# Kernel optimization log

Hardware: AMD Instinct MI355X
Metric: run time of the kernel (lower is better)

Reference implementation:

```python
import jax, jax.numpy as jnp
import numpy as np


def setup_inputs() -> dict:
    key = jax.random.key(0)
    k1, k2 = jax.random.split(key)
    n_nodes, d_feat, n_edges = 100000, 48, 1600000
    x = jax.random.normal(k1, (n_nodes, d_feat), dtype=jnp.float32)
    edge_index = jax.random.randint(k2, (2, n_edges), 0, n_nodes, dtype=jnp.int64)
    return {"x": x, "edge_index": edge_index, "batch_size": 65536}


def reference(x, edge_index, batch_size):
    # adj = SparseTensor.from_edge_index(edge_index): adj[row, col] = 1 with
    # row = edge_index[0] (src), col = edge_index[1] (dst).
    # adj.t() @ x  ->  out[i] = sum over edges (src -> i) of x[src]
    src, dst = edge_index[0], edge_index[1]
    n_nodes = x.shape[0]
    # memory-bound gather + scatter-add (SpMM, sum aggregation)
    x_neighbors_sum = jax.ops.segment_sum(x[src], dst, num_segments=n_nodes)
    node_labels = jnp.concatenate(
        (x[:batch_size, :], x_neighbors_sum[:batch_size, :]), axis=-1
    )
    return node_labels
```

## Files before the change

### kernel.cpp

```cpp
#include <hip/hip_runtime.h>
#include <hip/hip_fp16.h>

#define DFEAT 48
#define OUTW  96
#define NBINB 1024
#define BINTH 512
#define EPT   4
#define SORTCAP 2048
#define NBUCK2 512
#define RBITS 7
#define NROWS 128
#define RAWCAP 2560
#define CSRCAP 2560


static __device__ __forceinline__ unsigned short f2h(float f) {
    __half h = __float2half_rn(f);
    return *reinterpret_cast<unsigned short*>(&h);
}

static __device__ __forceinline__ int wave_iscan(int v, int lane) {
    #pragma unroll
    for (int d = 1; d < 64; d <<= 1) {
        int tv = __shfl_up(v, d, 64);
        if (lane >= d) v += tv;
    }
    return v;
}

__global__ __launch_bounds__(BINTH)
void bin_k(const int* __restrict__ ei, int n_edges, int batch, int chunk,
           const float4* __restrict__ x4, int nx4, uint2* __restrict__ xh4,
           unsigned short* __restrict__ starts, unsigned int* __restrict__ regions,
           float4* __restrict__ out4, int use_half) {
    __shared__ int cnt[NBUCK2];
    __shared__ int cur[NBUCK2];
    __shared__ int wsum[BINTH / 64];
    __shared__ int totS;
    __shared__ unsigned int sorted[SORTCAP];
    const int t = threadIdx.x;
    const int b = blockIdx.x;
    const int lane = t & 63, wid = t >> 6;

    if (use_half) {
        const int batch12 = batch * 12;
        for (int i = b * BINTH + t; i < nx4; i += NBINB * BINTH) {
            float4 v = x4[i];
            xh4[i] = make_uint2((unsigned)f2h(v.x) | ((unsigned)f2h(v.y) << 16),
                                (unsigned)f2h(v.z) | ((unsigned)f2h(v.w) << 16));
            if (i < batch12) {
                int row = i / 12, cg = i - row * 12;
                out4[(size_t)row * 24 + cg] = v;
            }
        }
    }

    const int beg = b * chunk;
    const int end = min(beg + chunk, n_edges);

    unsigned int pay[EPT];
    int bkt[EPT];
    #pragma unroll
    for (int i = 0; i < EPT; i++) {
        bkt[i] = -1;
        int e = beg + t + i * BINTH;
        if (e < end) {
            int dst = ei[n_edges + e];
            if (dst < batch) {
                int src = ei[e];
                bkt[i] = dst >> RBITS;
                pay[i] = ((unsigned)(dst & (NROWS - 1)) << 17) | (unsigned)src;
            }
        }
    }
    cnt[t] = 0;
    __syncthreads();
    #pragma unroll
    for (int i = 0; i < EPT; i++)
        if (bkt[i] >= 0) atomicAdd(&cnt[bkt[i]], 1);
    __syncthreads();
    int v = cnt[t];
    int iv = wave_iscan(v, lane);
    if (lane == 63) wsum[wid] = iv;
    __syncthreads();
    if (t < BINTH / 64) {
        int wv = wsum[t];
        int sv = wave_iscan(wv, t);
        wsum[t] = sv - wv;
        if (t == BINTH / 64 - 1) totS = sv;
    }
    __syncthreads();
    int excl = iv - v + wsum[wid];
    int tot = totS;
    cur[t] = excl;
    starts[t * NBINB + b] = (unsigned short)excl;
    if (t == 0) starts[NBUCK2 * NBINB + b] = (unsigned short)tot;
    __syncthreads();
    #pragma unroll
    for (int i = 0; i < EPT; i++)
        if (bkt[i] >= 0) {
            int pos = atomicAdd(&cur[bkt[i]], 1);
            sorted[pos] = pay[i];
        }
    __syncthreads();
    unsigned int* reg = regions + (size_t)b * chunk;
    for (int i = t; i < tot; i += BINTH) reg[i] = sorted[i];
}

__global__ __launch_bounds__(1024)
void reduce_k(const float* __restrict__ x, const uint4* __restrict__ xh4,
              const unsigned short* __restrict__ starts,
              const unsigned int* __restrict__ regions,
              float* __restrict__ out, int batch, int chunk, int use_half) {
    __shared__ unsigned int raw[RAWCAP];
    __shared__ int csr[CSRCAP];
    __shared__ int cnt[NROWS], off[NROWS + 1], cur[NROWS];
    __shared__ int rbase[NBINB], rs[NBINB], rl[NBINB];
    __shared__ int wsum[16];
    __shared__ int totS;
    const int t = threadIdx.x;
    const int kb = blockIdx.x;
    const int lane = t & 63, wid = t >> 6;

    int s0 = 0, len = 0;
    if (t < NBINB) {
        s0 = starts[kb * NBINB + t];
        int s1 = starts[(kb + 1) * NBINB + t];
        len = s1 - s0;
    }
    int iv = wave_iscan(len, lane);
    if (lane == 63 && wid < 16) wsum[wid] = iv;
    __syncthreads();
    if (t < 16) {
        int wv = wsum[t];
        int sv = wave_iscan(wv, t);
        wsum[t] = sv - wv;
        if (t == 15) totS = sv;
    }
    __syncthreads();
    if (t < NBINB) {
        rbase[t] = iv - len + wsum[wid];
        rs[t] = s0;
        rl[t] = len;
    }
    __syncthreads();
    const int T = min(totS, RAWCAP);
    {
        int r = t;
        if (r < NBINB) {
            int L = rl[r], base = rbase[r];
            const unsigned int* reg = regions + (size_t)r * chunk + rs[r];
            for (int idx = 0; idx < L; ++idx) {
                int p = base + idx;
                if (p < RAWCAP) raw[p] = reg[idx];
            }
        }
    }
    if (t < NROWS) cnt[t] = 0;
    __syncthreads();
    for (int i = t; i < T; i += 1024) atomicAdd(&cnt[raw[i] >> 17], 1);
    __syncthreads();
    int v2 = (t < NROWS) ? cnt[t] : 0;
    int iv2 = wave_iscan(v2, lane);
    if (lane == 63 && wid < 2) wsum[wid] = iv2;
    __syncthreads();
    if (t == 0) {
        int a = wsum[0];
        off[NROWS] = a + wsum[1];
        wsum[1] = a;
        wsum[0] = 0;
    }
    __syncthreads();
    if (t < NROWS) {
        int excl = iv2 - v2 + wsum[wid];
        off[t] = excl;
        cur[t] = excl;
    }
    __syncthreads();
    for (int i = t; i < T; i += 1024) {
        unsigned int p = raw[i];
        int pos = atomicAdd(&cur[p >> 17], 1);
        if (pos < CSRCAP) csr[pos] = (int)(p & 0x1FFFFu) * 6;
    }
    __syncthreads();

    if (use_half) {
        const int g   = lane / 6;
        const int cg  = lane - g * 6;
        const bool act = lane < 48;
        const bool isA = g < 4;
        const int gg  = isA ? g : g - 4;
        float4* out4 = (float4*)out;
        #pragma unroll
        for (int rr = 0; rr < 4; rr++) {
            const int ra = wid + 16 * rr;
            const int rb = ra + 64;
            const int rowA = kb * NROWS + ra;
            const int rowB = kb * NROWS + rb;
            const bool okA = rowA < batch, okB = rowB < batch;
            int e0a = 0, e1a = 0, e0b = 0, e1b = 0;
            if (okA) { e0a = off[ra]; e1a = min(off[ra + 1], CSRCAP); }
            if (okB) { e0b = off[rb]; e1b = min(off[rb + 1], CSRCAP); }
            const int e0 = isA ? e0a : e0b;
            const int e1 = isA ? e1a : e1b;
            float a0=0.f,a1=0.f,a2=0.f,a3=0.f,a4=0.f,a5=0.f,a6=0.f,a7=0.f;
            const int n = max(e1a - e0a, e1b - e0b);
            for (int k = 0; k < n; k += 16) {
                const int i1 = e0 + k + gg;
                const int i2 = i1 + 4;
                const int i3 = i1 + 8;
                const int i4 = i1 + 12;
                const bool v1 = act && i1 < e1;
                const bool v2 = act && i2 < e1;
                const bool v3 = act && i3 < e1;
                const bool v4 = act && i4 < e1;
                const int c1 = v1 ? csr[min(i1, CSRCAP - 1)] : 0;
                const int c2 = v2 ? csr[min(i2, CSRCAP - 1)] : 0;
                const int c3 = v3 ? csr[min(i3, CSRCAP - 1)] : 0;
                const int c4 = v4 ? csr[min(i4, CSRCAP - 1)] : 0;
                const uint4 p1 = xh4[(size_t)c1 + cg];
                const uint4 p2 = xh4[(size_t)c2 + cg];
                const uint4 p3 = xh4[(size_t)c3 + cg];
                const uint4 p4 = xh4[(size_t)c4 + cg];
                if (v1) {
                    float2 f0 = __half22float2(*(const __half2*)&p1.x);
                    float2 f1 = __half22float2(*(const __half2*)&p1.y);
                    float2 f2 = __half22float2(*(const __half2*)&p1.z);
                    float2 f3 = __half22float2(*(const __half2*)&p1.w);
                    a0 += f0.x; a1 += f0.y; a2 += f1.x; a3 += f1.y;
                    a4 += f2.x; a5 += f2.y; a6 += f3.x; a7 += f3.y;
                }
                if (v2) {
                    float2 f0 = __half22float2(*(const __half2*)&p2.x);
                    float2 f1 = __half22float2(*(const __half2*)&p2.y);
                    float2 f2 = __half22float2(*(const __half2*)&p2.z);
                    float2 f3 = __half22float2(*(const __half2*)&p2.w);
                    a0 += f0.x; a1 += f0.y; a2 += f1.x; a3 += f1.y;
                    a4 += f2.x; a5 += f2.y; a6 += f3.x; a7 += f3.y;
                }
                if (v3) {
                    float2 f0 = __half22float2(*(const __half2*)&p3.x);
                    float2 f1 = __half22float2(*(const __half2*)&p3.y);
                    float2 f2 = __half22float2(*(const __half2*)&p3.z);
                    float2 f3 = __half22float2(*(const __half2*)&p3.w);
                    a0 += f0.x; a1 += f0.y; a2 += f1.x; a3 += f1.y;
                    a4 += f2.x; a5 += f2.y; a6 += f3.x; a7 += f3.y;
                }
                if (v4) {
                    float2 f0 = __half22float2(*(const __half2*)&p4.x);
                    float2 f1 = __half22float2(*(const __half2*)&p4.y);
                    float2 f2 = __half22float2(*(const __half2*)&p4.z);
                    float2 f3 = __half22float2(*(const __half2*)&p4.w);
                    a0 += f0.x; a1 += f0.y; a2 += f1.x; a3 += f1.y;
                    a4 += f2.x; a5 += f2.y; a6 += f3.x; a7 += f3.y;
                }
            }
            float b0,b1,b2,b3,b4,b5,b6,b7;
            b0=__shfl(a0,lane+12); b1=__shfl(a1,lane+12);
            b2=__shfl(a2,lane+12); b3=__shfl(a3,lane+12);
            b4=__shfl(a4,lane+12); b5=__shfl(a5,lane+12);
            b6=__shfl(a6,lane+12); b7=__shfl(a7,lane+12);
            a0+=b0; a1+=b1; a2+=b2; a3+=b3; a4+=b4; a5+=b5; a6+=b6; a7+=b7;
            b0=__shfl(a0,lane+6); b1=__shfl(a1,lane+6);
            b2=__shfl(a2,lane+6); b3=__shfl(a3,lane+6);
            b4=__shfl(a4,lane+6); b5=__shfl(a5,lane+6);
            b6=__shfl(a6,lane+6); b7=__shfl(a7,lane+6);
            a0+=b0; a1+=b1; a2+=b2; a3+=b3; a4+=b4; a5+=b5; a6+=b6; a7+=b7;
            if (okA && lane < 6) {
                out4[(size_t)rowA * 24 + 12 + cg * 2]     = make_float4(a0,a1,a2,a3);
                out4[(size_t)rowA * 24 + 12 + cg * 2 + 1] = make_float4(a4,a5,a6,a7);
            }
            if (okB && lane >= 24 && lane < 30) {
                out4[(size_t)rowB * 24 + 12 + cg * 2]     = make_float4(a0,a1,a2,a3);
                out4[(size_t)rowB * 24 + 12 + cg * 2 + 1] = make_float4(a4,a5,a6,a7);
            }
        }
    } else {
        if (lane < DFEAT) {
            for (int r = wid; r < NROWS; r += 16) {
                int row = kb * NROWS + r;
                if (row >= batch) break;
                int e0 = off[r], e1 = min(off[r + 1], CSRCAP);
                float acc = 0.f;
                for (int e = e0; e < e1; ++e)
                    acc += x[(size_t)csr[e] * 8 + lane];
                out[(size_t)row * OUTW + lane]         = x[(size_t)row * DFEAT + lane];
                out[(size_t)row * OUTW + DFEAT + lane] = acc;
            }
        }
    }
}


#define D4   12
#define ROW4 24

__global__ void init_out_kernel(const float4* __restrict__ x4,
                                float4* __restrict__ out4, int batch) {
    int idx = blockIdx.x * blockDim.x + threadIdx.x;
    int total = batch * ROW4;
    if (idx >= total) return;
    int row = idx / ROW4;
    int c   = idx - row * ROW4;
    float4 v;
    if (c < D4) v = x4[row * D4 + c];
    else        v = make_float4(0.f, 0.f, 0.f, 0.f);
    out4[idx] = v;
}

__global__ void scatter_edges_kernel(const float4* __restrict__ x4,
                                     const int* __restrict__ ei,
                                     float* __restrict__ out,
                                     int n_edges, int batch) {
    int tid = blockIdx.x * blockDim.x + threadIdx.x;
    int e = tid / D4;
    int q = tid - e * D4;
    if (e >= n_edges) return;
    int dst = ei[n_edges + e];
    if (dst >= batch) return;
    int src = ei[e];
    float4 v = x4[src * D4 + q];
    float* p = out + (size_t)dst * OUTW + DFEAT + q * 4;
    atomicAdd(p + 0, v.x);
    atomicAdd(p + 1, v.y);
    atomicAdd(p + 2, v.z);
    atomicAdd(p + 3, v.w);
}


extern "C" void kernel_launch(void* const* d_in, const int* in_sizes, int n_in,
                              void* d_out, int out_size, void* d_ws, size_t ws_size,
                              hipStream_t stream) {
    const float* x  = (const float*)d_in[0];
    const int*   ei = (const int*)d_in[1];
    float* out = (float*)d_out;

    const int n_edges = in_sizes[1] / 2;
    const int batch   = out_size / OUTW;
    const int n_nodes = in_sizes[0] / DFEAT;
    const int chunk   = (n_edges + NBINB - 1) / NBINB;
    const int nbuck   = (batch + NROWS - 1) / NROWS;
    const int nx4     = n_nodes * DFEAT / 4;

    size_t xh_bytes = ((size_t)n_nodes * DFEAT * sizeof(unsigned short) + 15) & ~(size_t)15;
    size_t starts_bytes = (size_t)(NBUCK2 + 1) * NBINB * sizeof(unsigned short);
    size_t reg_bytes = (size_t)NBINB * chunk * sizeof(unsigned int);
    size_t need_h = xh_bytes + starts_bytes + reg_bytes;
    size_t need_f = starts_bytes + reg_bytes;

    bool base_ok = chunk <= SORTCAP && chunk <= BINTH * EPT && chunk < 65536 &&
                   n_nodes <= (1 << 17) && batch <= NBUCK2 * NROWS &&
                   (n_nodes * DFEAT) % 4 == 0 && nbuck >= 1 && nbuck <= NBUCK2 &&
                   batch % NROWS == 0;

    if (base_ok && ws_size >= need_h) {
        unsigned short* xh = (unsigned short*)d_ws;
        unsigned short* starts = (unsigned short*)((char*)d_ws + xh_bytes);
        unsigned int* regions = (unsigned int*)((char*)d_ws + xh_bytes + starts_bytes);
        bin_k<<<NBINB, BINTH, 0, stream>>>(ei, n_edges, batch, chunk,
                                           (const float4*)x, nx4, (uint2*)xh,
                                           starts, regions, (float4*)out, 1);
        reduce_k<<<nbuck, 1024, 0, stream>>>(x, (const uint4*)xh, starts, regions,
                                             out, batch, chunk, 1);
    } else if (base_ok && ws_size >= need_f) {
        unsigned short* starts = (unsigned short*)d_ws;
        unsigned int* regions = (unsigned int*)((char*)d_ws + starts_bytes);
        bin_k<<<NBINB, BINTH, 0, stream>>>(ei, n_edges, batch, chunk,
                                           (const float4*)x, nx4, (uint2*)0,
                                           starts, regions, (float4*)out, 0);
        reduce_k<<<nbuck, 1024, 0, stream>>>(x, (const uint4*)0, starts, regions,
                                             out, batch, chunk, 0);
    } else {
        {
            int total = batch * ROW4;
            int grid = (total + 255) / 256;
            init_out_kernel<<<grid, 256, 0, stream>>>((const float4*)x,
                                                      (float4*)out, batch);
        }
        {
            long long total = (long long)n_edges * D4;
            long long grid = (total + 255) / 256;
            scatter_edges_kernel<<<(int)grid, 256, 0, stream>>>(
                (const float4*)x, ei, out, n_edges, batch);
        }
    }
}
```

Measured before the change: 119.2 us.

## Bin edges into per-bucket global arenas via atomic cursors, halving bin blocks

The binning kernel now appends each bucket's sorted entries into a contiguous per-bucket global arena, reserving space with a global atomic cursor. It no longer writes per-block regions plus a starts table. The reduce kernel then reads one contiguous span instead of gathering 1024 small segments with a prefix scan. The bin grid is halved to 512 blocks with 7 edges per thread, and a memset of the cursors is added. Arena order is now nondeterministic, entries beyond RAWCAP are silently dropped, and the per-thread serial copy loop in bin_k may be uncoalesced.

```diff
diff --git a/kernel.cpp b/kernel.cpp
--- a/kernel.cpp
+++ b/kernel.cpp
@@ -3,15 +3,16 @@
 
 #define DFEAT 48
 #define OUTW  96
-#define NBINB 1024
+#define NBINB 512
 #define BINTH 512
-#define EPT   4
-#define SORTCAP 2048
+#define EPT   7
+#define SORTCAP 3584
 #define NBUCK2 512
 #define RBITS 7
 #define NROWS 128
 #define RAWCAP 2560
 #define CSRCAP 2560
+#define GSTRIDE 16
 
 
 static __device__ __forceinline__ unsigned short f2h(float f) {
@@ -31,12 +32,11 @@
 __global__ __launch_bounds__(BINTH)
 void bin_k(const int* __restrict__ ei, int n_edges, int batch, int chunk,
            const float4* __restrict__ x4, int nx4, uint2* __restrict__ xh4,
-           unsigned short* __restrict__ starts, unsigned int* __restrict__ regions,
+           unsigned int* __restrict__ gcur, unsigned int* __restrict__ arena,
            float4* __restrict__ out4, int use_half) {
     __shared__ int cnt[NBUCK2];
     __shared__ int cur[NBUCK2];
     __shared__ int wsum[BINTH / 64];
-    __shared__ int totS;
     __shared__ unsigned int sorted[SORTCAP];
     const int t = threadIdx.x;
     const int b = blockIdx.x;
@@ -87,14 +87,10 @@
         int wv = wsum[t];
         int sv = wave_iscan(wv, t);
         wsum[t] = sv - wv;
-        if (t == BINTH / 64 - 1) totS = sv;
     }
     __syncthreads();
     int excl = iv - v + wsum[wid];
-    int tot = totS;
     cur[t] = excl;
-    starts[t * NBINB + b] = (unsigned short)excl;
-    if (t == 0) starts[NBUCK2 * NBINB + b] = (unsigned short)tot;
     __syncthreads();
     #pragma unroll
     for (int i = 0; i < EPT; i++)
@@ -103,60 +99,33 @@
             sorted[pos] = pay[i];
         }
     __syncthreads();
-    unsigned int* reg = regions + (size_t)b * chunk;
-    for (int i = t; i < tot; i += BINTH) reg[i] = sorted[i];
+    if (v > 0) {
+        int gp = (int)atomicAdd(&gcur[t * GSTRIDE], (unsigned)v);
+        int lim = min(v, RAWCAP - gp);
+        unsigned int* dstp = arena + (size_t)t * RAWCAP + gp;
+        for (int i = 0; i < lim; i++) dstp[i] = sorted[excl + i];
+    }
 }
 
 __global__ __launch_bounds__(1024)
 void reduce_k(const float* __restrict__ x, const uint4* __restrict__ xh4,
-              const unsigned short* __restrict__ starts,
-              const unsigned int* __restrict__ regions,
-              float* __restrict__ out, int batch, int chunk, int use_half) {
+              const unsigned int* __restrict__ gcur,
+              const unsigned int* __restrict__ arena,
+              float* __restrict__ out, int batch, int use_half) {
     __shared__ unsigned int raw[RAWCAP];
     __shared__ int csr[CSRCAP];
     __shared__ int cnt[NROWS], off[NROWS + 1], cur[NROWS];
-    __shared__ int rbase[NBINB], rs[NBINB], rl[NBINB];
     __shared__ int wsum[16];
     __shared__ int totS;
     const int t = threadIdx.x;
     const int kb = blockIdx.x;
     const int lane = t & 63, wid = t >> 6;
 
-    int s0 = 0, len = 0;
-    if (t < NBINB) {
-        s0 = starts[kb * NBINB + t];
-        int s1 = starts[(kb + 1) * NBINB + t];
-        len = s1 - s0;
-    }
-    int iv = wave_iscan(len, lane);
-    if (lane == 63 && wid < 16) wsum[wid] = iv;
-    __syncthreads();
-    if (t < 16) {
-        int wv = wsum[t];
-        int sv = wave_iscan(wv, t);
-        wsum[t] = sv - wv;
-        if (t == 15) totS = sv;
-    }
-    __syncthreads();
-    if (t < NBINB) {
-        rbase[t] = iv - len + wsum[wid];
-        rs[t] = s0;
-        rl[t] = len;
-    }
-    __syncthreads();
-    const int T = min(totS, RAWCAP);
-    {
-        int r = t;
-        if (r < NBINB) {
-            int L = rl[r], base = rbase[r];
-            const unsigned int* reg = regions + (size_t)r * chunk + rs[r];
-            for (int idx = 0; idx < L; ++idx) {
-                int p = base + idx;
-                if (p < RAWCAP) raw[p] = reg[idx];
-            }
-        }
-    }
+    if (t == 0) totS = min((int)gcur[kb * GSTRIDE], RAWCAP);
     if (t < NROWS) cnt[t] = 0;
+    __syncthreads();
+    const int T = totS;
+    for (int i = t; i < T; i += 1024) raw[i] = arena[(size_t)kb * RAWCAP + i];
     __syncthreads();
     for (int i = t; i < T; i += 1024) atomicAdd(&cnt[raw[i] >> 17], 1);
     __syncthreads();
@@ -342,11 +311,11 @@
     const int nbuck   = (batch + NROWS - 1) / NROWS;
     const int nx4     = n_nodes * DFEAT / 4;
 
+    size_t gcur_bytes = (size_t)NBUCK2 * GSTRIDE * sizeof(unsigned int);
     size_t xh_bytes = ((size_t)n_nodes * DFEAT * sizeof(unsigned short) + 15) & ~(size_t)15;
-    size_t starts_bytes = (size_t)(NBUCK2 + 1) * NBINB * sizeof(unsigned short);
-    size_t reg_bytes = (size_t)NBINB * chunk * sizeof(unsigned int);
-    size_t need_h = xh_bytes + starts_bytes + reg_bytes;
-    size_t need_f = starts_bytes + reg_bytes;
+    size_t arena_bytes = (size_t)NBUCK2 * RAWCAP * sizeof(unsigned int);
+    size_t need_h = gcur_bytes + xh_bytes + arena_bytes;
+    size_t need_f = gcur_bytes + arena_bytes;
 
     bool base_ok = chunk <= SORTCAP && chunk <= BINTH * EPT && chunk < 65536 &&
                    n_nodes <= (1 << 17) && batch <= NBUCK2 * NROWS &&
@@ -354,22 +323,24 @@
                    batch % NROWS == 0;
 
     if (base_ok && ws_size >= need_h) {
-        unsigned short* xh = (unsigned short*)d_ws;
-        unsigned short* starts = (unsigned short*)((char*)d_ws + xh_bytes);
-        unsigned int* regions = (unsigned int*)((char*)d_ws + xh_bytes + starts_bytes);
+        unsigned int* gcur = (unsigned int*)d_ws;
+        unsigned short* xh = (unsigned short*)((char*)d_ws + gcur_bytes);
+        unsigned int* arena = (unsigned int*)((char*)d_ws + gcur_bytes + xh_bytes);
+        hipMemsetAsync(gcur, 0, gcur_bytes, stream);
         bin_k<<<NBINB, BINTH, 0, stream>>>(ei, n_edges, batch, chunk,
                                            (const float4*)x, nx4, (uint2*)xh,
-                                           starts, regions, (float4*)out, 1);
-        reduce_k<<<nbuck, 1024, 0, stream>>>(x, (const uint4*)xh, starts, regions,
-                                             out, batch, chunk, 1);
+                                           gcur, arena, (float4*)out, 1);
+        reduce_k<<<nbuck, 1024, 0, stream>>>(x, (const uint4*)xh, gcur, arena,
+                                             out, batch, 1);
     } else if (base_ok && ws_size >= need_f) {
-        unsigned short* starts = (unsigned short*)d_ws;
-        unsigned int* regions = (unsigned int*)((char*)d_ws + starts_bytes);
+        unsigned int* gcur = (unsigned int*)d_ws;
+        unsigned int* arena = (unsigned int*)((char*)d_ws + gcur_bytes);
+        hipMemsetAsync(gcur, 0, gcur_bytes, stream);
         bin_k<<<NBINB, BINTH, 0, stream>>>(ei, n_edges, batch, chunk,
                                            (const float4*)x, nx4, (uint2*)0,
-                                           starts, regions, (float4*)out, 0);
-        reduce_k<<<nbuck, 1024, 0, stream>>>(x, (const uint4*)0, starts, regions,
-                                             out, batch, chunk, 0);
+                                           gcur, arena, (float4*)out, 0);
+        reduce_k<<<nbuck, 1024, 0, stream>>>(x, (const uint4*)0, gcur, arena,
+                                             out, batch, 0);
     } else {
         {
             int total = batch * ROW4;
```

Measured after the change: 127.9 us. 7.3% more time.
